# Kernel tuning notes

Measured on AMD Instinct MI355X. Metric: run time of the kernel, lower is better.

Reference implementation:

```python
import jax, jax.numpy as jnp
import numpy as np

SEP = 2            # sep_token_id
B, S, H = 8, 4096, 768
MAX_SENT = 64      # = labels.size(1) in the original
STD = 0.02         # initializer_range


def setup_inputs() -> dict:
    key = jax.random.key(0)
    ks = jax.random.split(key, 6)
    hidden = jax.random.normal(ks[0], (B, S, H), jnp.float32)
    ids = jax.random.randint(ks[1], (B, S), 5, 30000, dtype=jnp.int64)
    # plant a sep every 64 tokens -> 64 seps, 64 non-empty sentences per row
    ids = ids.at[:, 63::64].set(SEP)
    W1 = jax.random.normal(ks[2], (H, 4096), jnp.float32) * STD
    b1 = jnp.zeros((4096,), jnp.float32)
    W2 = jax.random.normal(ks[3], (4096, 256), jnp.float32) * STD
    b2 = jnp.zeros((256,), jnp.float32)
    W3 = jax.random.normal(ks[4], (256, 2), jnp.float32) * STD
    b3 = jnp.zeros((2,), jnp.float32)
    return dict(hidden=hidden, input_ids=ids, W1=W1, b1=b1, W2=W2, b2=b2, W3=W3, b3=b3)


def _pool_row(h, ids):
    # h: [S, H], ids: [S] -> per-sentence means [MAX_SENT, H]
    sep = (ids == SEP)
    sep_i = sep.astype(jnp.int32)
    # exclusive cumsum: segment id = number of seps strictly before position t
    seg = jnp.cumsum(sep_i) - sep_i
    pos = jnp.arange(S)
    first_sep = jnp.argmax(sep)
    n_sep = sep_i.sum()
    # original includes the FIRST sep in sentence 0 but excludes later seps,
    # and excludes the last token of the trailing (post-last-sep) segment
    weight = jnp.where(sep, pos == first_sep, True)
    weight = weight & ~((pos == S - 1) & (seg == n_sep) & (n_sep > 0))
    # truncate to max_sentences: overflow segments land in a dump bucket
    seg_c = jnp.minimum(seg, MAX_SENT)
    hw = jnp.where(weight[:, None], h, 0.0)
    sums = jax.ops.segment_sum(hw, seg_c, num_segments=MAX_SENT + 1)[:MAX_SENT]
    cnts = jax.ops.segment_sum(weight.astype(h.dtype), seg_c, num_segments=MAX_SENT + 1)[:MAX_SENT]
    # empty (padding) segments -> zeros, matching the original zero-padding
    return jnp.where(cnts[:, None] > 0, sums / jnp.maximum(cnts, 1.0)[:, None], 0.0)


def reference(hidden, input_ids, W1, b1, W2, b2, W3, b3):
    # [B, MAX_SENT, H] per-sentence mean representations
    sent = jax.vmap(_pool_row)(hidden, input_ids)
    # classifier head (dropout = identity in eval); GELU is exact (torch nn.GELU default)
    x = jax.nn.gelu(jnp.einsum('bmh,hf->bmf', sent, W1) + b1, approximate=False)
    x = jax.nn.gelu(jnp.einsum('bmf,fg->bmg', x, W2) + b2, approximate=False)
    logits = jnp.einsum('bmg,gc->bmc', x, W3) + b3  # [B, MAX_SENT, 2]
    return logits
```

## Files before the change

### kernel.cpp

```cpp
#include <hip/hip_runtime.h>
#include <hip/hip_bf16.h>

#define SEP_ID 2
#define S_LEN  4096
#define HID    768
#define MAXS   64

using short8  = __attribute__((ext_vector_type(8))) short;
using floatx4 = __attribute__((ext_vector_type(4))) float;

__device__ __forceinline__ float gelu_exact(float x) {
    return 0.5f * x * (1.0f + erff(x * 0.70710678118654752f));
}

__global__ __launch_bounds__(256) void prep_kernel(const int* __restrict__ ids,
                                                   const float* __restrict__ W1,
                                                   const float* __restrict__ W2,
                                                   __hip_bfloat16* __restrict__ W1T,
                                                   __hip_bfloat16* __restrict__ W2T,
                                                   int* __restrict__ sent_start,
                                                   int* __restrict__ sent_cnt) {
    __shared__ __align__(16) char smem[16896];
    const int blk = blockIdx.x;
    const int t = threadIdx.x;

    if (blk < 8) {
        int* sep_pos = (int*)smem;
        int* wtot    = sep_pos + 4096;
        const int b = blk;
        const int* row = ids + (size_t)b * S_LEN;
        const int lane = t & 63, w = t >> 6;

        int local[16]; int c = 0;
        const int base = t * 16;
        #pragma unroll
        for (int q = 0; q < 4; ++q) {
            int4 v = ((const int4*)row)[t * 4 + q];
            if (v.x == SEP_ID) local[c++] = base + q * 4 + 0;
            if (v.y == SEP_ID) local[c++] = base + q * 4 + 1;
            if (v.z == SEP_ID) local[c++] = base + q * 4 + 2;
            if (v.w == SEP_ID) local[c++] = base + q * 4 + 3;
        }
        int scan = c;
        #pragma unroll
        for (int off = 1; off < 64; off <<= 1) {
            int n = __shfl_up(scan, off);
            if (lane >= off) scan += n;
        }
        if (lane == 63) wtot[w] = scan;
        __syncthreads();
        int wbase = 0;
        for (int i = 0; i < w; ++i) wbase += wtot[i];
        const int o = wbase + scan - c;
        for (int i = 0; i < c; ++i) sep_pos[o + i] = local[i];
        __syncthreads();
        const int n_sep = wtot[0] + wtot[1] + wtot[2] + wtot[3];

        if (t < MAXS) {
            const int m = t;
            int start = 0, cnt = 0;
            if (n_sep == 0) {
                if (m == 0) { start = 0; cnt = S_LEN; }
            } else if (m < n_sep) {
                if (m == 0) { start = 0; cnt = sep_pos[0] + 1; }
                else { start = sep_pos[m - 1] + 1; cnt = sep_pos[m] - sep_pos[m - 1] - 1; }
            } else if (m == n_sep) {
                start = sep_pos[n_sep - 1] + 1;
                cnt = (S_LEN - 1) - start;
                if (cnt < 0) cnt = 0;
            }
            sent_start[b * MAXS + m] = start;
            sent_cnt[b * MAXS + m]  = cnt;
        }
    } else {
        float* tile = (float*)smem;
        const int id0 = blk - 8;
        const float* in; __hip_bfloat16* outw; int K, N, n0, k0;
        if (id0 < 3072) { in = W1; outw = W1T; K = 768;  N = 4096;
                          n0 = (id0 & 127) * 32; k0 = (id0 >> 7) * 32; }
        else { const int id = id0 - 3072;
               in = W2; outw = W2T; K = 4096; N = 256;
               n0 = (id & 7) * 32; k0 = (id >> 3) * 32; }
        const int c = t & 31;
        const int r = t >> 5;
        #pragma unroll
        for (int i = 0; i < 32; i += 8)
            tile[(r + i) * 33 + c] = in[(size_t)(k0 + r + i) * N + n0 + c];
        __syncthreads();
        #pragma unroll
        for (int i = 0; i < 32; i += 8)
            outw[(size_t)(n0 + r + i) * K + k0 + c] = __float2bfloat16(tile[c * 33 + r + i]);
    }
}

__global__ __launch_bounds__(192) void pool_kernel(const float* __restrict__ hidden,
                                                   const int* __restrict__ sent_start,
                                                   const int* __restrict__ sent_cnt,
                                                   __hip_bfloat16* __restrict__ sent) {
    const int blk = blockIdx.x;
    const int b = blk >> 6;
    const int t = threadIdx.x;
    const int start = sent_start[blk];
    const int cnt   = sent_cnt[blk];

    const float4* base = (const float4*)(hidden + ((size_t)b * S_LEN + start) * HID);
    float ax = 0.f, ay = 0.f, az = 0.f, aw = 0.f;
    int i = 0;
    for (; i + 8 <= cnt; i += 8) {
        float4 v[8];
        #pragma unroll
        for (int j = 0; j < 8; ++j) v[j] = base[(size_t)(i + j) * 192 + t];
        #pragma unroll
        for (int j = 0; j < 8; ++j) { ax += v[j].x; ay += v[j].y; az += v[j].z; aw += v[j].w; }
    }
    for (; i < cnt; ++i) {
        float4 v = base[(size_t)i * 192 + t];
        ax += v.x; ay += v.y; az += v.z; aw += v.w;
    }
    const float inv = (cnt > 0) ? 1.0f / (float)cnt : 0.0f;
    __hip_bfloat16* o = sent + (size_t)blk * HID + t * 4;
    o[0] = __float2bfloat16(ax * inv);
    o[1] = __float2bfloat16(ay * inv);
    o[2] = __float2bfloat16(az * inv);
    o[3] = __float2bfloat16(aw * inv);
}

__global__ __launch_bounds__(256) void gemm1_kernel(const __hip_bfloat16* __restrict__ A,
                                                    const __hip_bfloat16* __restrict__ BT,
                                                    const float* __restrict__ bias,
                                                    __hip_bfloat16* __restrict__ out) {
    const int n0 = blockIdx.x * 64;
    const int m0 = blockIdx.y * 64;
    const int t = threadIdx.x;
    const int w = t >> 6, l = t & 63;
    const int wm = (w >> 1) * 32;
    const int wn = (w & 1) * 32;

    __shared__ __hip_bfloat16 Al[64][72];
    __shared__ __hip_bfloat16 Bl[64][72];

    floatx4 acc[2][2] = {};

    const int r  = t >> 2;
    const int ch = (t & 3) * 16;
    const __hip_bfloat16* Ag = A  + (size_t)(m0 + r) * 768 + ch;
    const __hip_bfloat16* Bg = BT + (size_t)(n0 + r) * 768 + ch;

    const int lr = l & 15;
    const int kq = (l >> 4) * 8;

    for (int k0 = 0; k0 < 768; k0 += 64) {
        short8 av0 = *(const short8*)(Ag + k0);
        short8 av1 = *(const short8*)(Ag + k0 + 8);
        short8 bv0 = *(const short8*)(Bg + k0);
        short8 bv1 = *(const short8*)(Bg + k0 + 8);
        __syncthreads();
        *(short8*)(&Al[r][ch])     = av0;
        *(short8*)(&Al[r][ch + 8]) = av1;
        *(short8*)(&Bl[r][ch])     = bv0;
        *(short8*)(&Bl[r][ch + 8]) = bv1;
        __syncthreads();

        #pragma unroll
        for (int ks = 0; ks < 64; ks += 32) {
            short8 a0 = *(const short8*)(&Al[wm + lr][ks + kq]);
            short8 a1 = *(const short8*)(&Al[wm + 16 + lr][ks + kq]);
            short8 b0 = *(const short8*)(&Bl[wn + lr][ks + kq]);
            short8 b1 = *(const short8*)(&Bl[wn + 16 + lr][ks + kq]);
            acc[0][0] = __builtin_amdgcn_mfma_f32_16x16x32_bf16(a0, b0, acc[0][0], 0, 0, 0);
            acc[0][1] = __builtin_amdgcn_mfma_f32_16x16x32_bf16(a0, b1, acc[0][1], 0, 0, 0);
            acc[1][0] = __builtin_amdgcn_mfma_f32_16x16x32_bf16(a1, b0, acc[1][0], 0, 0, 0);
            acc[1][1] = __builtin_amdgcn_mfma_f32_16x16x32_bf16(a1, b1, acc[1][1], 0, 0, 0);
        }
    }

    #pragma unroll
    for (int i = 0; i < 2; ++i) {
        #pragma unroll
        for (int j = 0; j < 2; ++j) {
            const int col  = n0 + wn + j * 16 + lr;
            const int rowb = m0 + wm + i * 16 + (l >> 4) * 4;
            const float bv = bias[col];
            #pragma unroll
            for (int rg = 0; rg < 4; ++rg) {
                float x = acc[i][j][rg] + bv;
                out[(size_t)(rowb + rg) * 4096 + col] = __float2bfloat16(gelu_exact(x));
            }
        }
    }
}

__global__ __launch_bounds__(256) void gemm2_kernel(const __hip_bfloat16* __restrict__ A,
                                                    const __hip_bfloat16* __restrict__ BT,
                                                    float* __restrict__ part) {
    const int n0 = blockIdx.x * 64;
    const int m0 = blockIdx.y * 64;
    const int s  = blockIdx.z;
    const int kb = s * 256;
    const int t = threadIdx.x;
    const int w = t >> 6, l = t & 63;
    const int wm = (w >> 1) * 32;
    const int wn = (w & 1) * 32;

    __shared__ __hip_bfloat16 Al[64][72];
    __shared__ __hip_bfloat16 Bl[64][72];

    floatx4 acc[2][2] = {};

    const int r  = t >> 2;
    const int ch = (t & 3) * 16;
    const __hip_bfloat16* Ag = A  + (size_t)(m0 + r) * 4096 + kb + ch;
    const __hip_bfloat16* Bg = BT + (size_t)(n0 + r) * 4096 + kb + ch;

    const int lr = l & 15;
    const int kq = (l >> 4) * 8;

    for (int k0 = 0; k0 < 256; k0 += 64) {
        short8 av0 = *(const short8*)(Ag + k0);
        short8 av1 = *(const short8*)(Ag + k0 + 8);
        short8 bv0 = *(const short8*)(Bg + k0);
        short8 bv1 = *(const short8*)(Bg + k0 + 8);
        __syncthreads();
        *(short8*)(&Al[r][ch])     = av0;
        *(short8*)(&Al[r][ch + 8]) = av1;
        *(short8*)(&Bl[r][ch])     = bv0;
        *(short8*)(&Bl[r][ch + 8]) = bv1;
        __syncthreads();

        #pragma unroll
        for (int ks = 0; ks < 64; ks += 32) {
            short8 a0 = *(const short8*)(&Al[wm + lr][ks + kq]);
            short8 a1 = *(const short8*)(&Al[wm + 16 + lr][ks + kq]);
            short8 b0 = *(const short8*)(&Bl[wn + lr][ks + kq]);
            short8 b1 = *(const short8*)(&Bl[wn + 16 + lr][ks + kq]);
            acc[0][0] = __builtin_amdgcn_mfma_f32_16x16x32_bf16(a0, b0, acc[0][0], 0, 0, 0);
            acc[0][1] = __builtin_amdgcn_mfma_f32_16x16x32_bf16(a0, b1, acc[0][1], 0, 0, 0);
            acc[1][0] = __builtin_amdgcn_mfma_f32_16x16x32_bf16(a1, b0, acc[1][0], 0, 0, 0);
            acc[1][1] = __builtin_amdgcn_mfma_f32_16x16x32_bf16(a1, b1, acc[1][1], 0, 0, 0);
        }
    }

    float* po = part + (size_t)s * 512 * 256;
    #pragma unroll
    for (int i = 0; i < 2; ++i) {
        #pragma unroll
        for (int j = 0; j < 2; ++j) {
            const int col  = n0 + wn + j * 16 + lr;
            const int rowb = m0 + wm + i * 16 + (l >> 4) * 4;
            #pragma unroll
            for (int rg = 0; rg < 4; ++rg)
                po[(size_t)(rowb + rg) * 256 + col] = acc[i][j][rg];
        }
    }
}

__global__ __launch_bounds__(256) void rh_kernel(const float* __restrict__ part,
                                                 const float* __restrict__ b2,
                                                 const float* __restrict__ W3,
                                                 const float* __restrict__ b3,
                                                 float* __restrict__ out) {
    const int row = blockIdx.x;
    const int c = threadIdx.x;
    const int w = c >> 6, l = c & 63;

    float s = 0.f;
    #pragma unroll
    for (int k = 0; k < 16; ++k)
        s += part[((size_t)k * 512 + row) * 256 + c];
    const float x = gelu_exact(s + b2[c]);
    float y0 = x * W3[c * 2 + 0];
    float y1 = x * W3[c * 2 + 1];
    #pragma unroll
    for (int off = 32; off; off >>= 1) {
        y0 += __shfl_down(y0, off);
        y1 += __shfl_down(y1, off);
    }
    __shared__ float r0[4], r1[4];
    if (l == 0) { r0[w] = y0; r1[w] = y1; }
    __syncthreads();
    if (c == 0) out[row * 2 + 0] = r0[0] + r0[1] + r0[2] + r0[3] + b3[0];
    if (c == 1) out[row * 2 + 1] = r1[0] + r1[1] + r1[2] + r1[3] + b3[1];
}

extern "C" void kernel_launch(void* const* d_in, const int* in_sizes, int n_in,
                              void* d_out, int out_size, void* d_ws, size_t ws_size,
                              hipStream_t stream) {
    const float* hidden = (const float*)d_in[0];
    const int*   ids    = (const int*)d_in[1];
    const float* W1     = (const float*)d_in[2];
    const float* b1     = (const float*)d_in[3];
    const float* W2     = (const float*)d_in[4];
    const float* b2     = (const float*)d_in[5];
    const float* W3     = (const float*)d_in[6];
    const float* b3     = (const float*)d_in[7];
    float* out = (float*)d_out;

    char* ws = (char*)d_ws;
    int* sent_start        = (int*)(ws + 0);
    int* sent_cnt          = (int*)(ws + 2048);
    __hip_bfloat16* sentb  = (__hip_bfloat16*)(ws + 4096);
    __hip_bfloat16* W1T    = (__hip_bfloat16*)(ws + 790528);
    __hip_bfloat16* W2T    = (__hip_bfloat16*)(ws + 7081984);
    __hip_bfloat16* x1     = (__hip_bfloat16*)(ws + 9179136);
    float* part            = (float*)(ws + 13373440);

    prep_kernel<<<4104, 256, 0, stream>>>(ids, W1, W2, W1T, W2T, sent_start, sent_cnt);
    pool_kernel<<<512, 192, 0, stream>>>(hidden, sent_start, sent_cnt, sentb);
    gemm1_kernel<<<dim3(64, 8), 256, 0, stream>>>(sentb, W1T, b1, x1);
    gemm2_kernel<<<dim3(4, 8, 16), 256, 0, stream>>>(x1, W2T, part);
    rh_kernel<<<512, 256, 0, stream>>>(part, b2, W3, b3, out);
}
```

Baseline: 199.0 us.

## Fuse sentence pooling into prep kernel, recomputing sep scan per sentence block

Merges the pooling kernel into the prep kernel. Each of 512 blocks now redoes the separator scan for its row and then pools its own sentence, so the separate sentence start/count buffers and one kernel launch go away. The pooling now runs concurrently with the weight transpose/convert blocks in the same grid. The cost is that every sentence block rereads its 16KB ids row and repeats the scan, 64x redundant work per row, and only 192 of 256 threads do the pooling.

```diff
diff --git a/kernel.cpp b/kernel.cpp
--- a/kernel.cpp
+++ b/kernel.cpp
@@ -13,21 +13,22 @@
     return 0.5f * x * (1.0f + erff(x * 0.70710678118654752f));
 }
 
-__global__ __launch_bounds__(256) void prep_kernel(const int* __restrict__ ids,
-                                                   const float* __restrict__ W1,
-                                                   const float* __restrict__ W2,
-                                                   __hip_bfloat16* __restrict__ W1T,
-                                                   __hip_bfloat16* __restrict__ W2T,
-                                                   int* __restrict__ sent_start,
-                                                   int* __restrict__ sent_cnt) {
-    __shared__ __align__(16) char smem[16896];
+__global__ __launch_bounds__(256) void stage1_kernel(const int* __restrict__ ids,
+                                                     const float* __restrict__ hidden,
+                                                     const float* __restrict__ W1,
+                                                     const float* __restrict__ W2,
+                                                     __hip_bfloat16* __restrict__ W1T,
+                                                     __hip_bfloat16* __restrict__ W2T,
+                                                     __hip_bfloat16* __restrict__ sentb) {
+    __shared__ __align__(16) char smem[16640];
     const int blk = blockIdx.x;
     const int t = threadIdx.x;
 
-    if (blk < 8) {
+    if (blk < 512) {
         int* sep_pos = (int*)smem;
         int* wtot    = sep_pos + 4096;
-        const int b = blk;
+        const int sidx = blk;
+        const int b = sidx >> 6, m = sidx & 63;
         const int* row = ids + (size_t)b * S_LEN;
         const int lane = t & 63, w = t >> 6;
 
@@ -56,25 +57,43 @@
         __syncthreads();
         const int n_sep = wtot[0] + wtot[1] + wtot[2] + wtot[3];
 
-        if (t < MAXS) {
-            const int m = t;
-            int start = 0, cnt = 0;
-            if (n_sep == 0) {
-                if (m == 0) { start = 0; cnt = S_LEN; }
-            } else if (m < n_sep) {
-                if (m == 0) { start = 0; cnt = sep_pos[0] + 1; }
-                else { start = sep_pos[m - 1] + 1; cnt = sep_pos[m] - sep_pos[m - 1] - 1; }
-            } else if (m == n_sep) {
-                start = sep_pos[n_sep - 1] + 1;
-                cnt = (S_LEN - 1) - start;
-                if (cnt < 0) cnt = 0;
+        int start = 0, cnt = 0;
+        if (n_sep == 0) {
+            if (m == 0) { start = 0; cnt = S_LEN; }
+        } else if (m < n_sep) {
+            if (m == 0) { start = 0; cnt = sep_pos[0] + 1; }
+            else { start = sep_pos[m - 1] + 1; cnt = sep_pos[m] - sep_pos[m - 1] - 1; }
+        } else if (m == n_sep) {
+            start = sep_pos[n_sep - 1] + 1;
+            cnt = (S_LEN - 1) - start;
+            if (cnt < 0) cnt = 0;
+        }
+
+        if (t < 192) {
+            const float4* bp = (const float4*)(hidden + ((size_t)b * S_LEN + start) * HID);
+            float ax = 0.f, ay = 0.f, az = 0.f, aw = 0.f;
+            int i = 0;
+            for (; i + 8 <= cnt; i += 8) {
+                float4 v[8];
+                #pragma unroll
+                for (int j = 0; j < 8; ++j) v[j] = bp[(size_t)(i + j) * 192 + t];
+                #pragma unroll
+                for (int j = 0; j < 8; ++j) { ax += v[j].x; ay += v[j].y; az += v[j].z; aw += v[j].w; }
             }
-            sent_start[b * MAXS + m] = start;
-            sent_cnt[b * MAXS + m]  = cnt;
+            for (; i < cnt; ++i) {
+                float4 v = bp[(size_t)i * 192 + t];
+                ax += v.x; ay += v.y; az += v.z; aw += v.w;
+            }
+            const float inv = (cnt > 0) ? 1.0f / (float)cnt : 0.0f;
+            __hip_bfloat16* o2 = sentb + (size_t)sidx * HID + t * 4;
+            o2[0] = __float2bfloat16(ax * inv);
+            o2[1] = __float2bfloat16(ay * inv);
+            o2[2] = __float2bfloat16(az * inv);
+            o2[3] = __float2bfloat16(aw * inv);
         }
     } else {
         float* tile = (float*)smem;
-        const int id0 = blk - 8;
+        const int id0 = blk - 512;
         const float* in; __hip_bfloat16* outw; int K, N, n0, k0;
         if (id0 < 3072) { in = W1; outw = W1T; K = 768;  N = 4096;
                           n0 = (id0 & 127) * 32; k0 = (id0 >> 7) * 32; }
@@ -91,38 +110,6 @@
         for (int i = 0; i < 32; i += 8)
             outw[(size_t)(n0 + r + i) * K + k0 + c] = __float2bfloat16(tile[c * 33 + r + i]);
     }
-}
-
-__global__ __launch_bounds__(192) void pool_kernel(const float* __restrict__ hidden,
-                                                   const int* __restrict__ sent_start,
-                                                   const int* __restrict__ sent_cnt,
-                                                   __hip_bfloat16* __restrict__ sent) {
-    const int blk = blockIdx.x;
-    const int b = blk >> 6;
-    const int t = threadIdx.x;
-    const int start = sent_start[blk];
-    const int cnt   = sent_cnt[blk];
-
-    const float4* base = (const float4*)(hidden + ((size_t)b * S_LEN + start) * HID);
-    float ax = 0.f, ay = 0.f, az = 0.f, aw = 0.f;
-    int i = 0;
-    for (; i + 8 <= cnt; i += 8) {
-        float4 v[8];
-        #pragma unroll
-        for (int j = 0; j < 8; ++j) v[j] = base[(size_t)(i + j) * 192 + t];
-        #pragma unroll
-        for (int j = 0; j < 8; ++j) { ax += v[j].x; ay += v[j].y; az += v[j].z; aw += v[j].w; }
-    }
-    for (; i < cnt; ++i) {
-        float4 v = base[(size_t)i * 192 + t];
-        ax += v.x; ay += v.y; az += v.z; aw += v.w;
-    }
-    const float inv = (cnt > 0) ? 1.0f / (float)cnt : 0.0f;
-    __hip_bfloat16* o = sent + (size_t)blk * HID + t * 4;
-    o[0] = __float2bfloat16(ax * inv);
-    o[1] = __float2bfloat16(ay * inv);
-    o[2] = __float2bfloat16(az * inv);
-    o[3] = __float2bfloat16(aw * inv);
 }
 
 __global__ __launch_bounds__(256) void gemm1_kernel(const __hip_bfloat16* __restrict__ A,
@@ -296,16 +283,13 @@
     float* out = (float*)d_out;
 
     char* ws = (char*)d_ws;
-    int* sent_start        = (int*)(ws + 0);
-    int* sent_cnt          = (int*)(ws + 2048);
-    __hip_bfloat16* sentb  = (__hip_bfloat16*)(ws + 4096);
-    __hip_bfloat16* W1T    = (__hip_bfloat16*)(ws + 790528);
-    __hip_bfloat16* W2T    = (__hip_bfloat16*)(ws + 7081984);
-    __hip_bfloat16* x1     = (__hip_bfloat16*)(ws + 9179136);
-    float* part            = (float*)(ws + 13373440);
-
-    prep_kernel<<<4104, 256, 0, stream>>>(ids, W1, W2, W1T, W2T, sent_start, sent_cnt);
-    pool_kernel<<<512, 192, 0, stream>>>(hidden, sent_start, sent_cnt, sentb);
+    __hip_bfloat16* sentb  = (__hip_bfloat16*)(ws + 0);
+    __hip_bfloat16* W1T    = (__hip_bfloat16*)(ws + 786432);
+    __hip_bfloat16* W2T    = (__hip_bfloat16*)(ws + 7077888);
+    __hip_bfloat16* x1     = (__hip_bfloat16*)(ws + 9175040);
+    float* part            = (float*)(ws + 13369344);
+
+    stage1_kernel<<<4608, 256, 0, stream>>>(ids, hidden, W1, W2, W1T, W2T, sentb);
     gemm1_kernel<<<dim3(64, 8), 256, 0, stream>>>(sentb, W1T, b1, x1);
     gemm2_kernel<<<dim3(4, 8, 16), 256, 0, stream>>>(x1, W2T, part);
     rh_kernel<<<512, 256, 0, stream>>>(part, b2, W3, b3, out);
```

Result: no change. 195.4 us (-1.8%).
